# Kernel optimization log

Hardware: AMD Instinct MI355X
Metric: run time of the kernel (lower is better)

The kernel has to match this reference:

```python
import jax, jax.numpy as jnp
import numpy as np

B, S, DIM = 1, 2048, 4096
NH, NKV, HD = 32, 8, 128
REPEATS = NH // NKV
ROPE_THETA = 10000.0


def setup_inputs() -> dict:
    key = jax.random.key(0)
    ks = jax.random.split(key, 6)
    x = jax.random.normal(ks[0], (B, S, DIM), jnp.float32) * 0.02
    wq = jax.random.normal(ks[1], (NH * HD, DIM), jnp.float32) * 0.02
    wk = jax.random.normal(ks[2], (NKV * HD, DIM), jnp.float32) * 0.02
    wv = jax.random.normal(ks[3], (NKV * HD, DIM), jnp.float32) * 0.02
    wo = jax.random.normal(ks[4], (DIM, NH * HD), jnp.float32) * 0.02
    # rotary frequencies (real cos/sin form of complex freqs_cis)
    inv_freq = 1.0 / (ROPE_THETA ** (jnp.arange(0, HD, 2, dtype=jnp.float32) / HD))
    ang = jnp.arange(S, dtype=jnp.float32)[:, None] * inv_freq[None, :]  # [S, HD//2]
    freqs_cos = jnp.cos(ang)
    freqs_sin = jnp.sin(ang)
    positions = jnp.arange(S, dtype=jnp.int32)  # prompt phase: all positions
    # additive causal mask
    mask = jnp.where(jnp.tril(jnp.ones((S, S), bool)), 0.0, -1e9).astype(jnp.float32)
    cache_k = jnp.zeros((B, S, NKV, HD), jnp.float32)
    cache_v = jnp.zeros((B, S, NKV, HD), jnp.float32)
    return dict(x=x, wq=wq, wk=wk, wv=wv, wo=wo, freqs_cos=freqs_cos,
                freqs_sin=freqs_sin, cache_k=cache_k, cache_v=cache_v,
                positions=positions, mask=mask)


def apply_rope(t, cos, sin):
    # t: [b, s, h, d]; pairs are (d0,d1),(d2,d3),... matching view_as_complex
    tr = t[..., 0::2]
    ti = t[..., 1::2]
    c = cos[None, :, None, :]
    s = sin[None, :, None, :]
    out_r = tr * c - ti * s
    out_i = tr * s + ti * c
    return jnp.stack([out_r, out_i], axis=-1).reshape(t.shape)


def reference(x, wq, wk, wv, wo, freqs_cos, freqs_sin, cache_k, cache_v, positions, mask):
    b, s, _ = x.shape
    xq = jnp.einsum('bsd,od->bso', x, wq).reshape(b, s, NH, HD)
    xk = jnp.einsum('bsd,od->bso', x, wk).reshape(b, s, NKV, HD)
    xv = jnp.einsum('bsd,od->bso', x, wv).reshape(b, s, NKV, HD)
    xq = apply_rope(xq, freqs_cos, freqs_sin)
    xk = apply_rope(xk, freqs_cos, freqs_sin)
    # KV-cache scatter (prompt phase writes; output uses fresh xk/xv here)
    cache_k = cache_k.at[:, positions].set(xk)
    cache_v = cache_v.at[:, positions].set(xv)
    # GQA: repeat_interleave kv heads to match query heads
    k = jnp.repeat(xk, REPEATS, axis=2).transpose(0, 2, 1, 3)  # [b, NH, s, HD]
    v = jnp.repeat(xv, REPEATS, axis=2).transpose(0, 2, 1, 3)
    q = xq.transpose(0, 2, 1, 3)
    scale = HD ** -0.5
    scores = jnp.einsum('bhqd,bhkd->bhqk', q, k) * scale + mask[None, None]
    probs = jax.nn.softmax(scores.astype(jnp.float32), axis=-1).astype(q.dtype)
    out = jnp.einsum('bhqk,bhkd->bhqd', probs, v)
    out = out.transpose(0, 2, 1, 3).reshape(b, s, NH * HD)
    return jnp.einsum('bso,do->bsd', out, wo)
```

## Files before the change

kernel.cpp:

```cpp
#include <hip/hip_runtime.h>
#include <hip/hip_bf16.h>
#include <stdint.h>

typedef __bf16 bf16_t;
typedef __attribute__((ext_vector_type(8))) __bf16 bf16x8;
typedef __attribute__((ext_vector_type(4))) float f32x4;
typedef __attribute__((ext_vector_type(8))) unsigned short u16x8;

#define S_LEN 2048
#define DIM   4096
#define QKVN  6144
#define NHEAD 32
#define HDIM  128

typedef __attribute__((address_space(1))) unsigned int as1_u32;
typedef __attribute__((address_space(3))) unsigned int as3_u32;

__device__ __forceinline__ unsigned short f2bf(float f) {
  unsigned u = __builtin_bit_cast(unsigned, f);
  u += 0x7fffu + ((u >> 16) & 1u);
  return (unsigned short)(u >> 16);
}

__device__ __forceinline__ void gload_lds16(const void* g, void* l) {
  __builtin_amdgcn_global_load_lds(
      (as1_u32*)(unsigned long long)(uintptr_t)g,
      (as3_u32*)(unsigned int)(uintptr_t)l,
      16, 0, 0);
}

__global__ __launch_bounds__(256) void cvt5_kernel(const float* __restrict__ x,
                                                   const float* __restrict__ wq,
                                                   const float* __restrict__ wk,
                                                   const float* __restrict__ wv,
                                                   const float* __restrict__ wo,
                                                   ushort4* __restrict__ xb,
                                                   ushort4* __restrict__ wqkvb,
                                                   ushort4* __restrict__ wob) {
  const long N0 = 2097152;
  const long N1 = N0 + 4194304;
  const long N2 = N1 + 1048576;
  const long N3 = N2 + 1048576;
  const long N4 = N3 + 4194304;
  long idx = (long)blockIdx.x * 256 + threadIdx.x;
  long stride = (long)gridDim.x * 256;
  for (long i = idx; i < N4; i += stride) {
    const float4* s; ushort4* d; long o;
    if (i < N0)      { s = (const float4*)x;  d = xb;              o = i; }
    else if (i < N1) { s = (const float4*)wq; d = wqkvb;           o = i - N0; }
    else if (i < N2) { s = (const float4*)wk; d = wqkvb + 4194304; o = i - N1; }
    else if (i < N3) { s = (const float4*)wv; d = wqkvb + 5242880; o = i - N2; }
    else             { s = (const float4*)wo; d = wob;             o = i - N3; }
    float4 v = s[o];
    ushort4 r;
    r.x = f2bf(v.x); r.y = f2bf(v.y); r.z = f2bf(v.z); r.w = f2bf(v.w);
    d[o] = r;
  }
}

__device__ __forceinline__ bf16x8 fld(const char* half, int row, int chunk) {
  return *(const bf16x8*)(half + row * 128 + ((chunk ^ (row & 7)) << 4));
}

__device__ __forceinline__ void mfma8(const bf16x8 (*af)[2], const bf16x8 (*bf_)[2],
                                      f32x4 (*acc)[4], int mbase, int nbase) {
#pragma unroll
  for (int m = 0; m < 4; ++m)
#pragma unroll
    for (int n = 0; n < 2; ++n) {
      acc[mbase + m][nbase + n] = __builtin_amdgcn_mfma_f32_16x16x32_bf16(
          af[mbase + m][0], bf_[nbase + n][0], acc[mbase + m][nbase + n], 0, 0, 0);
      acc[mbase + m][nbase + n] = __builtin_amdgcn_mfma_f32_16x16x32_bf16(
          af[mbase + m][1], bf_[nbase + n][1], acc[mbase + m][nbase + n], 0, 0, 0);
    }
}

template <int OUTF32>
__global__ __launch_bounds__(512, 2) void gemm8p(const bf16_t* __restrict__ A,
                                                 const bf16_t* __restrict__ B,
                                                 void* __restrict__ Cout,
                                                 int M, int N, int K, int nxt) {
  __shared__ char lds[131072];
  const int tid = threadIdx.x;
  const int lane = tid & 63, w = tid >> 6;
  const int wm = w >> 2, wn = w & 3;
  const int lg = lane >> 4, lr = lane & 15;
  const int nwg = gridDim.x;
  const int orig = blockIdx.x;
  const int wgid = (orig & 7) * (nwg >> 3) + (orig >> 3);
  const int bx = wgid % nxt, by = wgid / nxt;
  const long rowA = (long)by * 256;
  const long rowB = (long)bx * 256;

  f32x4 acc[8][4];
  const f32x4 z4 = {0.f, 0.f, 0.f, 0.f};
#pragma unroll
  for (int i = 0; i < 8; ++i)
#pragma unroll
    for (int j = 0; j < 4; ++j) acc[i][j] = z4;

  const int r0 = tid >> 3, sl = tid & 7;
  const long xo  = (long)((sl ^ (r0 & 7)) << 3);
  const long aof = (rowA + r0) * (long)K + xo;
  const long bof = (rowB + r0) * (long)K + xo;
  const long j1  = (long)64 * K;
  const long h1  = (long)128 * K;
  const int ld0 = tid * 16, ld1 = (tid + 512) * 16;

#define STG_A(K0, HALF, DBUF)                                                  \
  { char* hp = lds + (DBUF) * 65536 + (HALF) * 16384;                          \
    gload_lds16(A + aof + (HALF) * h1 + (K0),      hp + ld0);                  \
    gload_lds16(A + aof + (HALF) * h1 + j1 + (K0), hp + ld1); }
#define STG_B(K0, HALF, DBUF)                                                  \
  { char* hp = lds + (DBUF) * 65536 + 32768 + (HALF) * 16384;                  \
    gload_lds16(B + bof + (HALF) * h1 + (K0),      hp + ld0);                  \
    gload_lds16(B + bof + (HALF) * h1 + j1 + (K0), hp + ld1); }

  const int nt = K >> 6;
  const int bro = (wn & 1) * 64;

  STG_A(0, 0, 0); STG_A(0, 1, 0); STG_B(0, 0, 0); STG_B(0, 1, 0);
  STG_B(64, 0, 1); STG_B(64, 1, 1);
  asm volatile("s_waitcnt vmcnt(4)" ::: "memory");
  __builtin_amdgcn_s_barrier();

  bf16x8 af[8][2], bf_[4][2];

  for (int t = 0; t < nt; ++t) {
    const int d = t & 1;
    const char* Ah = lds + d * 65536 + wm * 16384;
    const char* Bh = lds + d * 65536 + 32768 + (wn >> 1) * 16384;
    const int k1 = (t + 1) << 6, k2 = (t + 2) << 6;
#pragma unroll
    for (int m = 0; m < 4; ++m) {
      af[m][0] = fld(Ah, m * 16 + lr, lg);
      af[m][1] = fld(Ah, m * 16 + lr, 4 + lg);
    }
#pragma unroll
    for (int n = 0; n < 2; ++n) {
      bf_[n][0] = fld(Bh, bro + n * 16 + lr, lg);
      bf_[n][1] = fld(Bh, bro + n * 16 + lr, 4 + lg);
    }
    if (t + 1 < nt) STG_A(k1, 0, d ^ 1);
    __builtin_amdgcn_s_barrier();
    asm volatile("s_waitcnt lgkmcnt(0)" ::: "memory");
    __builtin_amdgcn_sched_barrier(0);
    __builtin_amdgcn_s_setprio(1);
    mfma8(af, bf_, acc, 0, 0);
    __builtin_amdgcn_s_setprio(0);
    __builtin_amdgcn_s_barrier();
#pragma unroll
    for (int n = 2; n < 4; ++n) {
      bf_[n][0] = fld(Bh, bro + n * 16 + lr, lg);
      bf_[n][1] = fld(Bh, bro + n * 16 + lr, 4 + lg);
    }
    if (t + 1 < nt) STG_A(k1, 1, d ^ 1);
    __builtin_amdgcn_s_barrier();
    asm volatile("s_waitcnt lgkmcnt(0)" ::: "memory");
    __builtin_amdgcn_sched_barrier(0);
    __builtin_amdgcn_s_setprio(1);
    mfma8(af, bf_, acc, 0, 2);
    __builtin_amdgcn_s_setprio(0);
    __builtin_amdgcn_s_barrier();
#pragma unroll
    for (int m = 4; m < 8; ++m) {
      af[m][0] = fld(Ah, m * 16 + lr, lg);
      af[m][1] = fld(Ah, m * 16 + lr, 4 + lg);
    }
    if (t + 2 < nt) STG_B(k2, 0, d);
    __builtin_amdgcn_s_barrier();
    asm volatile("s_waitcnt lgkmcnt(0)" ::: "memory");
    __builtin_amdgcn_sched_barrier(0);
    __builtin_amdgcn_s_setprio(1);
    mfma8(af, bf_, acc, 4, 0);
    __builtin_amdgcn_s_setprio(0);
    __builtin_amdgcn_s_barrier();
    if (t + 2 < nt) STG_B(k2, 1, d);
    __builtin_amdgcn_s_barrier();
    __builtin_amdgcn_s_setprio(1);
    mfma8(af, bf_, acc, 4, 2);
    __builtin_amdgcn_s_setprio(0);
    if (t + 2 < nt) {
      asm volatile("s_waitcnt vmcnt(4)" ::: "memory");
    } else {
      asm volatile("s_waitcnt vmcnt(0)" ::: "memory");
    }
    __builtin_amdgcn_s_barrier();
  }
#undef STG_A
#undef STG_B

  const long crow = rowA + wm * 128;
  const long ccol = rowB + wn * 64;
  if (OUTF32) {
    float* C = (float*)Cout;
#pragma unroll
    for (int mf = 0; mf < 8; ++mf)
#pragma unroll
      for (int j = 0; j < 4; ++j) {
        long row = crow + mf * 16 + lg * 4 + j;
        float* cp = C + row * N + ccol + lr;
#pragma unroll
        for (int nf = 0; nf < 4; ++nf) cp[nf * 16] = acc[mf][nf][j];
      }
  } else {
    unsigned short* C = (unsigned short*)Cout;
#pragma unroll
    for (int mf = 0; mf < 8; ++mf)
#pragma unroll
      for (int j = 0; j < 4; ++j) {
        long row = crow + mf * 16 + lg * 4 + j;
        unsigned short* cp = C + row * N + ccol + lr;
#pragma unroll
        for (int nf = 0; nf < 4; ++nf) cp[nf * 16] = f2bf(acc[mf][nf][j]);
      }
  }
}

__global__ __launch_bounds__(256) void rope_kernel(unsigned int* __restrict__ qkv32,
                                                   const float* __restrict__ cosb,
                                                   const float* __restrict__ sinb) {
  int t = blockIdx.x * 256 + threadIdx.x;
  int i  = t & 63;
  int sh = t >> 6;
  int hh = sh % 40;
  int s  = sh / 40;
  int col2 = (hh < 32) ? (hh * 64 + i) : (2048 + (hh - 32) * 64 + i);
  unsigned int* p = qkv32 + (long)s * (QKVN / 2) + col2;
  unsigned int v = *p;
  float tr = __builtin_bit_cast(float, (v & 0xffffu) << 16);
  float ti = __builtin_bit_cast(float, v & 0xffff0000u);
  float c  = cosb[s * 64 + i];
  float sn = sinb[s * 64 + i];
  float orr = tr * c - ti * sn;
  float oi  = tr * sn + ti * c;
  *p = (unsigned int)f2bf(orr) | ((unsigned int)f2bf(oi) << 16);
}

__global__ __launch_bounds__(256) void vtrans_kernel(const bf16_t* __restrict__ qkv,
                                                     bf16_t* __restrict__ vT) {
  const int kh = blockIdx.x;
  const int hd = threadIdx.x & 127;
  const int s0 = blockIdx.y * 16 + (threadIdx.x >> 7) * 8;
  u16x8 v;
#pragma unroll
  for (int e = 0; e < 8; ++e)
    v[e] = *(const unsigned short*)(qkv + (long)(s0 + e) * QKVN + 5120 + kh * HDIM + hd);
  *(u16x8*)(vT + ((long)kh * HDIM + hd) * S_LEN + s0) = v;
}

__global__ __launch_bounds__(512) void attn_kernel(const bf16_t* __restrict__ qkv,
                                                   const bf16_t* __restrict__ vT,
                                                   unsigned short* __restrict__ ob) {
  __shared__ bf16_t Kt[64 * 128];
  __shared__ bf16_t Vt[128 * 64];
  __shared__ bf16_t Pl[8 * 16 * 64];
  const int h  = blockIdx.x;
  const int qi = 15 - (int)blockIdx.y;
  const int qb = qi * 128;
  const int kh = h >> 2;
  const int tid = threadIdx.x, lane = tid & 63, w = tid >> 6;
  const int lg = lane >> 4, lr = lane & 15;
  const int qrow0 = qb + w * 16;

  bf16x8 qf[4];
  const bf16_t* qptr = qkv + (long)(qrow0 + lr) * QKVN + h * HDIM + lg * 8;
#pragma unroll
  for (int kk = 0; kk < 4; ++kk) qf[kk] = *(const bf16x8*)(qptr + kk * 32);

  const f32x4 z4 = {0.f, 0.f, 0.f, 0.f};
  f32x4 oacc[8];
#pragma unroll
  for (int c = 0; c < 8; ++c) oacc[c] = z4;
  float m[4]    = {-1e30f, -1e30f, -1e30f, -1e30f};
  float lsum[4] = {0.f, 0.f, 0.f, 0.f};

  char* KtB = (char*)Kt;
  char* VtB = (char*)Vt;
  char* PlB = (char*)Pl + w * 2048;
  const float scale = 0.08838834764831845f;
  const int ntiles = 2 * qi + 2;
  const int wqmax = qrow0 + 15;

  for (int t = 0; t < ntiles; ++t) {
    const int kv0 = t * 64;
    __syncthreads();
#pragma unroll
    for (int it = 0; it < 2; ++it) {
      int cch = tid + it * 512;
      int r = cch >> 4, c = cch & 15;
      const bf16_t* src = qkv + (long)(kv0 + r) * QKVN + 4096 + kh * HDIM
                          + ((c ^ (r & 7)) * 8);
      gload_lds16(src, KtB + cch * 16);
    }
#pragma unroll
    for (int it = 0; it < 2; ++it) {
      int cch = tid + it * 512;
      int hd = cch >> 3, c = cch & 7;
      const bf16_t* src = vT + ((long)kh * HDIM + hd) * S_LEN + kv0
                          + ((c ^ (hd & 7)) * 8);
      gload_lds16(src, VtB + cch * 16);
    }
    __syncthreads();
    if (kv0 > wqmax) continue;

    f32x4 sf[4];
#pragma unroll
    for (int f = 0; f < 4; ++f) {
      f32x4 a = z4;
      int n = f * 16 + lr;
      int rb = n * 256, sw = (n & 7) << 4;
#pragma unroll
      for (int kk = 0; kk < 4; ++kk) {
        bf16x8 kf = *(const bf16x8*)(KtB + rb + (((kk * 4 + lg) * 16) ^ sw));
        a = __builtin_amdgcn_mfma_f32_16x16x32_bf16(qf[kk], kf, a, 0, 0, 0);
      }
      sf[f] = a;
    }

    float sc_arr[4];
#pragma unroll
    for (int j = 0; j < 4; ++j) {
      int qrow = qrow0 + lg * 4 + j;
      float sv[4];
#pragma unroll
      for (int f = 0; f < 4; ++f) {
        float s = sf[f][j] * scale;
        if (kv0 + f * 16 + lr > qrow) s = -1e9f;
        sv[f] = s;
      }
      float mx = fmaxf(fmaxf(sv[0], sv[1]), fmaxf(sv[2], sv[3]));
      mx = fmaxf(mx, __shfl_xor(mx, 1));
      mx = fmaxf(mx, __shfl_xor(mx, 2));
      mx = fmaxf(mx, __shfl_xor(mx, 4));
      mx = fmaxf(mx, __shfl_xor(mx, 8));
      float mn = fmaxf(m[j], mx);
      float p[4];
#pragma unroll
      for (int f = 0; f < 4; ++f) p[f] = __expf(sv[f] - mn);
      float ps = (p[0] + p[1]) + (p[2] + p[3]);
      ps += __shfl_xor(ps, 1);
      ps += __shfl_xor(ps, 2);
      ps += __shfl_xor(ps, 4);
      ps += __shfl_xor(ps, 8);
      float sc = __expf(m[j] - mn);
      lsum[j] = lsum[j] * sc + ps;
      m[j] = mn;
      sc_arr[j] = sc;
      int row = lg * 4 + j;
      int swp = (row & 7) << 4;
#pragma unroll
      for (int f = 0; f < 4; ++f)
        *(unsigned short*)(PlB + row * 128 + (((f * 16 + lr) * 2) ^ swp)) = f2bf(p[f]);
    }
#pragma unroll
    for (int c = 0; c < 8; ++c)
#pragma unroll
      for (int j = 0; j < 4; ++j) oacc[c][j] *= sc_arr[j];

    bf16x8 pfr[2];
#pragma unroll
    for (int kk = 0; kk < 2; ++kk)
      pfr[kk] = *(const bf16x8*)(PlB + lr * 128 + (((kk * 4 + lg) * 16) ^ ((lr & 7) << 4)));
#pragma unroll
    for (int c = 0; c < 8; ++c) {
      int hd = c * 16 + lr;
      int rb = hd * 128, sw = (hd & 7) << 4;
#pragma unroll
      for (int kk = 0; kk < 2; ++kk) {
        bf16x8 vf = *(const bf16x8*)(VtB + rb + (((kk * 4 + lg) * 16) ^ sw));
        oacc[c] = __builtin_amdgcn_mfma_f32_16x16x32_bf16(pfr[kk], vf, oacc[c], 0, 0, 0);
      }
    }
  }

  float rl[4];
#pragma unroll
  for (int j = 0; j < 4; ++j) rl[j] = 1.f / lsum[j];
#pragma unroll
  for (int c = 0; c < 8; ++c)
#pragma unroll
    for (int j = 0; j < 4; ++j) {
      long row = qrow0 + lg * 4 + j;
      ob[row * 4096 + h * 128 + c * 16 + lr] = f2bf(oacc[c][j] * rl[j]);
    }
}

extern "C" void kernel_launch(void* const* d_in, const int* in_sizes, int n_in,
                              void* d_out, int out_size, void* d_ws, size_t ws_size,
                              hipStream_t stream) {
  const float* x  = (const float*)d_in[0];
  const float* wq = (const float*)d_in[1];
  const float* wk = (const float*)d_in[2];
  const float* wv = (const float*)d_in[3];
  const float* wo = (const float*)d_in[4];
  const float* fc = (const float*)d_in[5];
  const float* fs = (const float*)d_in[6];

  char* ws = (char*)d_ws;
  bf16_t* xb    = (bf16_t*)(ws + 0);
  bf16_t* wqkvb = (bf16_t*)(ws + 16777216);
  bf16_t* wob   = (bf16_t*)(ws + 67108864);
  bf16_t* qkv   = (bf16_t*)(ws + 100663296);
  bf16_t* ob    = (bf16_t*)(ws + 125829120);
  bf16_t* vT    = (bf16_t*)(ws + 0);

  cvt5_kernel<<<2048, 256, 0, stream>>>(x, wq, wk, wv, wo,
                                        (ushort4*)xb, (ushort4*)wqkvb, (ushort4*)wob);

  gemm8p<0><<<192, 512, 0, stream>>>(xb, wqkvb, qkv, 2048, 6144, 4096, 24);
  vtrans_kernel<<<dim3(8, 128), 256, 0, stream>>>(qkv, vT);
  rope_kernel<<<20480, 256, 0, stream>>>((unsigned int*)qkv, fc, fs);
  attn_kernel<<<dim3(32, 16), 512, 0, stream>>>(qkv, vT, (unsigned short*)ob);
  gemm8p<1><<<128, 512, 0, stream>>>(ob, wob, d_out, 2048, 4096, 4096, 16);
}
```

Measured before the change: 359.7 us.

## Use 256x128-tile GEMM kernel with two blocks per CU for output projection

Adds a new GEMM kernel gemm8r that uses a 256x128 output tile (half the N width of gemm8p), 96KB LDS, and launch bounds allowing two 512-thread blocks per CU. The output projection now launches 256 blocks instead of 128, so the 256 CUs of the device are all occupied instead of half. A staged pipeline interleaves LDS fragment loads, async global-to-LDS prefetch and MFMA quadrants with barriers and setprio. The cost is lower data reuse per tile and more barriers per k-step.

New measurement: 330.1 us. 8.2% less time.

```diff
diff --git a/kernel.cpp b/kernel.cpp
--- a/kernel.cpp
+++ b/kernel.cpp
@@ -217,6 +217,169 @@
   }
 }
 
+template <int OUTF32>
+__global__ __launch_bounds__(512, 2) void gemm8r(const bf16_t* __restrict__ A,
+                                                 const bf16_t* __restrict__ B,
+                                                 void* __restrict__ Cout,
+                                                 int M, int N, int K, int nxt) {
+  __shared__ char lds[98304];
+  const int tid = threadIdx.x;
+  const int lane = tid & 63, w = tid >> 6;
+  const int wm = w >> 1, wn = w & 1;
+  const int lg = lane >> 4, lr = lane & 15;
+  const int nwg = gridDim.x;
+  const int orig = blockIdx.x;
+  const int wgid = (orig & 7) * (nwg >> 3) + (orig >> 3);
+  const int bx = wgid % nxt, by = wgid / nxt;
+  const long rowA = (long)by * 256;
+  const long rowB = (long)bx * 128;
+
+  f32x4 acc[4][4];
+  const f32x4 z4 = {0.f, 0.f, 0.f, 0.f};
+#pragma unroll
+  for (int i = 0; i < 4; ++i)
+#pragma unroll
+    for (int j = 0; j < 4; ++j) acc[i][j] = z4;
+
+  const int r0 = tid >> 3, sl = tid & 7;
+  const long xo  = (long)((sl ^ (r0 & 7)) << 3);
+  const long aof = (rowA + r0) * (long)K + xo;
+  const long bof = (rowB + r0) * (long)K + xo;
+  const long r64 = (long)64 * K;
+  const int ld0 = tid * 16, ld1 = (tid + 512) * 16;
+
+#define RSTG_A(K0, HALF, DBUF)                                                 \
+  { char* ap = lds + (DBUF) * 49152 + (HALF) * 16384;                          \
+    gload_lds16(A + aof + (HALF) * 2 * r64 + (K0),       ap + ld0);            \
+    gload_lds16(A + aof + (HALF) * 2 * r64 + r64 + (K0), ap + ld1); }
+#define RSTG_B(K0, DBUF)                                                       \
+  { char* bp = lds + (DBUF) * 49152 + 32768;                                   \
+    gload_lds16(B + bof + (K0),       bp + ld0);                               \
+    gload_lds16(B + bof + r64 + (K0), bp + ld1); }
+
+  const int nt = K >> 6;
+
+  RSTG_A(0, 0, 0); RSTG_A(0, 1, 0); RSTG_B(0, 0);
+  RSTG_B(64, 1);
+  asm volatile("s_waitcnt vmcnt(2)" ::: "memory");
+  __builtin_amdgcn_s_barrier();
+
+  bf16x8 af[4][2], bf_[4][2];
+
+  for (int t = 0; t < nt; ++t) {
+    const int d = t & 1;
+    const char* Ar = lds + d * 49152;
+    const char* Br = Ar + 32768;
+    const int arow = wm * 64, brow = wn * 64;
+    const int k1 = (t + 1) << 6, k2 = (t + 2) << 6;
+#pragma unroll
+    for (int m = 0; m < 2; ++m) {
+      af[m][0] = fld(Ar, arow + m * 16 + lr, lg);
+      af[m][1] = fld(Ar, arow + m * 16 + lr, 4 + lg);
+    }
+#pragma unroll
+    for (int n = 0; n < 2; ++n) {
+      bf_[n][0] = fld(Br, brow + n * 16 + lr, lg);
+      bf_[n][1] = fld(Br, brow + n * 16 + lr, 4 + lg);
+    }
+    if (t + 1 < nt) RSTG_A(k1, 0, d ^ 1);
+    __builtin_amdgcn_s_barrier();
+    asm volatile("s_waitcnt lgkmcnt(0)" ::: "memory");
+    __builtin_amdgcn_sched_barrier(0);
+    __builtin_amdgcn_s_setprio(1);
+#pragma unroll
+    for (int m = 0; m < 2; ++m)
+#pragma unroll
+      for (int n = 0; n < 2; ++n) {
+        acc[m][n] = __builtin_amdgcn_mfma_f32_16x16x32_bf16(af[m][0], bf_[n][0], acc[m][n], 0, 0, 0);
+        acc[m][n] = __builtin_amdgcn_mfma_f32_16x16x32_bf16(af[m][1], bf_[n][1], acc[m][n], 0, 0, 0);
+      }
+    __builtin_amdgcn_s_setprio(0);
+    __builtin_amdgcn_s_barrier();
+#pragma unroll
+    for (int n = 2; n < 4; ++n) {
+      bf_[n][0] = fld(Br, brow + n * 16 + lr, lg);
+      bf_[n][1] = fld(Br, brow + n * 16 + lr, 4 + lg);
+    }
+    if (t + 1 < nt) RSTG_A(k1, 1, d ^ 1);
+    __builtin_amdgcn_s_barrier();
+    asm volatile("s_waitcnt lgkmcnt(0)" ::: "memory");
+    __builtin_amdgcn_sched_barrier(0);
+    __builtin_amdgcn_s_setprio(1);
+#pragma unroll
+    for (int m = 0; m < 2; ++m)
+#pragma unroll
+      for (int n = 2; n < 4; ++n) {
+        acc[m][n] = __builtin_amdgcn_mfma_f32_16x16x32_bf16(af[m][0], bf_[n][0], acc[m][n], 0, 0, 0);
+        acc[m][n] = __builtin_amdgcn_mfma_f32_16x16x32_bf16(af[m][1], bf_[n][1], acc[m][n], 0, 0, 0);
+      }
+    __builtin_amdgcn_s_setprio(0);
+    __builtin_amdgcn_s_barrier();
+#pragma unroll
+    for (int m = 2; m < 4; ++m) {
+      af[m][0] = fld(Ar, arow + m * 16 + lr, lg);
+      af[m][1] = fld(Ar, arow + m * 16 + lr, 4 + lg);
+    }
+    if (t + 2 < nt) RSTG_B(k2, d);
+    __builtin_amdgcn_s_barrier();
+    asm volatile("s_waitcnt lgkmcnt(0)" ::: "memory");
+    __builtin_amdgcn_sched_barrier(0);
+    __builtin_amdgcn_s_setprio(1);
+#pragma unroll
+    for (int m = 2; m < 4; ++m)
+#pragma unroll
+      for (int n = 0; n < 2; ++n) {
+        acc[m][n] = __builtin_amdgcn_mfma_f32_16x16x32_bf16(af[m][0], bf_[n][0], acc[m][n], 0, 0, 0);
+        acc[m][n] = __builtin_amdgcn_mfma_f32_16x16x32_bf16(af[m][1], bf_[n][1], acc[m][n], 0, 0, 0);
+      }
+    __builtin_amdgcn_s_setprio(0);
+    __builtin_amdgcn_s_barrier();
+    __builtin_amdgcn_s_setprio(1);
+#pragma unroll
+    for (int m = 2; m < 4; ++m)
+#pragma unroll
+      for (int n = 2; n < 4; ++n) {
+        acc[m][n] = __builtin_amdgcn_mfma_f32_16x16x32_bf16(af[m][0], bf_[n][0], acc[m][n], 0, 0, 0);
+        acc[m][n] = __builtin_amdgcn_mfma_f32_16x16x32_bf16(af[m][1], bf_[n][1], acc[m][n], 0, 0, 0);
+      }
+    __builtin_amdgcn_s_setprio(0);
+    if (t + 2 < nt) {
+      asm volatile("s_waitcnt vmcnt(2)" ::: "memory");
+    } else {
+      asm volatile("s_waitcnt vmcnt(0)" ::: "memory");
+    }
+    __builtin_amdgcn_s_barrier();
+  }
+#undef RSTG_A
+#undef RSTG_B
+
+  const long crow = rowA + wm * 64;
+  const long ccol = rowB + wn * 64;
+  if (OUTF32) {
+    float* C = (float*)Cout;
+#pragma unroll
+    for (int mf = 0; mf < 4; ++mf)
+#pragma unroll
+      for (int j = 0; j < 4; ++j) {
+        long row = crow + mf * 16 + lg * 4 + j;
+        float* cp = C + row * N + ccol + lr;
+#pragma unroll
+        for (int nf = 0; nf < 4; ++nf) cp[nf * 16] = acc[mf][nf][j];
+      }
+  } else {
+    unsigned short* C = (unsigned short*)Cout;
+#pragma unroll
+    for (int mf = 0; mf < 4; ++mf)
+#pragma unroll
+      for (int j = 0; j < 4; ++j) {
+        long row = crow + mf * 16 + lg * 4 + j;
+        unsigned short* cp = C + row * N + ccol + lr;
+#pragma unroll
+        for (int nf = 0; nf < 4; ++nf) cp[nf * 16] = f2bf(acc[mf][nf][j]);
+      }
+  }
+}
+
 __global__ __launch_bounds__(256) void rope_kernel(unsigned int* __restrict__ qkv32,
                                                    const float* __restrict__ cosb,
                                                    const float* __restrict__ sinb) {
@@ -412,5 +575,5 @@
   vtrans_kernel<<<dim3(8, 128), 256, 0, stream>>>(qkv, vT);
   rope_kernel<<<20480, 256, 0, stream>>>((unsigned int*)qkv, fc, fs);
   attn_kernel<<<dim3(32, 16), 512, 0, stream>>>(qkv, vT, (unsigned short*)ob);
-  gemm8p<1><<<128, 512, 0, stream>>>(ob, wob, d_out, 2048, 4096, 4096, 16);
-}
+  gemm8r<1><<<256, 512, 0, stream>>>(ob, wob, d_out, 2048, 4096, 4096, 32);
+}
```
